# Performance work log

Measured on AMD Instinct MI355X. Metric: run time of the kernel, lower is better.

Reference implementation:

```python
import jax, jax.numpy as jnp
import numpy as np

D_MODEL = 512


def setup_inputs() -> dict:
    key = jax.random.key(0)
    ks = jax.random.split(key, 9)
    B, S, D = 2, 4096, D_MODEL
    scale = 1.0 / np.sqrt(D)
    return {
        "Q": jax.random.normal(ks[0], (B, S, D), dtype=jnp.float32),
        "K": jax.random.normal(ks[1], (B, S, D), dtype=jnp.float32),
        "V": jax.random.normal(ks[2], (B, S, D), dtype=jnp.float32),
        "W_q": jax.random.normal(ks[3], (D, D), dtype=jnp.float32) * scale,
        "b_q": jax.random.normal(ks[4], (D,), dtype=jnp.float32) * scale,
        "W_k": jax.random.normal(ks[5], (D, D), dtype=jnp.float32) * scale,
        "b_k": jax.random.normal(ks[6], (D,), dtype=jnp.float32) * scale,
        "W_v": jax.random.normal(ks[7], (D, D), dtype=jnp.float32) * scale,
        "b_v": jax.random.normal(ks[8], (D,), dtype=jnp.float32) * scale,
    }


def reference(Q, K, V, W_q, b_q, W_k, b_k, W_v, b_v):
    # Linear projections (torch Linear: x @ W.T + b)
    q = jnp.einsum("bsd,ed->bse", Q, W_q) + b_q  # [B,S,D]
    k = jnp.einsum("bsd,ed->bse", K, W_k) + b_k
    v = jnp.einsum("bsd,ed->bse", V, W_v) + b_v
    d_k = k.shape[-1]
    scores = jnp.einsum("bqd,bkd->bqk", q, k) / jnp.sqrt(jnp.asarray(d_k, q.dtype))
    attn = jax.nn.softmax(scores, axis=-1)  # [B,S,S]
    return jnp.einsum("bqk,bkd->bqd", attn, v)
```

## Files before the change

kernel.cpp:

```cpp
#include <hip/hip_runtime.h>
#include <hip/hip_bf16.h>
#include <math.h>
#include <stdint.h>

typedef __attribute__((ext_vector_type(8))) short short8;
typedef __attribute__((ext_vector_type(4))) float floatx4;
typedef __attribute__((ext_vector_type(4))) unsigned short ushort4v;

__device__ __forceinline__ void gload_lds16(const void* g, void* lds) {
    __builtin_amdgcn_global_load_lds(
        (__attribute__((address_space(1))) void*)(g),
        (__attribute__((address_space(3))) void*)(lds), 16, 0, 0);
}
__device__ __forceinline__ float bf16bits_to_f(unsigned short u) {
    union { unsigned int i; float f; } x; x.i = ((unsigned int)u) << 16; return x.f;
}
__device__ __forceinline__ unsigned short f_to_bf16bits(float f) {
    union { float f; unsigned int i; } x; x.f = f;
    unsigned int lsb = (x.i >> 16) & 1u;
    x.i += 0x7fffu + lsb;
    return (unsigned short)(x.i >> 16);
}

__global__ __launch_bounds__(256) void conv1_kernel(
    const float4* __restrict__ in, ushort4v* __restrict__ out)
{
    const int i = blockIdx.x * 256 + threadIdx.x;
    float4 v = in[i];
    ushort4v o;
    o[0] = f_to_bf16bits(v.x); o[1] = f_to_bf16bits(v.y);
    o[2] = f_to_bf16bits(v.z); o[3] = f_to_bf16bits(v.w);
    out[i] = o;
}

__global__ __launch_bounds__(256) void conv_wb_kernel(
    const float* __restrict__ Wq, const float* __restrict__ Wk, const float* __restrict__ Wv,
    const float* __restrict__ bq, const float* __restrict__ bk, const float* __restrict__ bv,
    unsigned short* __restrict__ Wo,
    unsigned short* __restrict__ bo)
{
    const int m = blockIdx.y;
    const float* W = (m == 0) ? Wq : (m == 1) ? Wk : Wv;
    const float* b = (m == 0) ? bq : (m == 1) ? bk : bv;
    if (blockIdx.x < 256) {
        const int idx = (blockIdx.x * 256 + threadIdx.x) * 4;
        float4 v = *(const float4*)&W[idx];
        ushort4v o;
        o[0] = f_to_bf16bits(v.x); o[1] = f_to_bf16bits(v.y);
        o[2] = f_to_bf16bits(v.z); o[3] = f_to_bf16bits(v.w);
        *(ushort4v*)&Wo[(size_t)m * 262144 + idx] = o;
    } else if (threadIdx.x < 128) {
        const int idx = threadIdx.x * 4;
        float4 v = *(const float4*)&b[idx];
        ushort4v o;
        o[0] = f_to_bf16bits(v.x); o[1] = f_to_bf16bits(v.y);
        o[2] = f_to_bf16bits(v.z); o[3] = f_to_bf16bits(v.w);
        *(ushort4v*)&bo[(size_t)m * 512 + idx] = o;
    }
}

__global__ __launch_bounds__(256, 2) void proj_kernel(
    const unsigned short* __restrict__ X,
    const unsigned short* __restrict__ W,
    const unsigned short* __restrict__ bias,
    unsigned short* __restrict__ qbuf,
    unsigned short* __restrict__ kbuf,
    unsigned short* __restrict__ vTbuf,
    int mode, float qscale)
{
    __shared__ __align__(16) unsigned short Xs[128 * 64];
    __shared__ __align__(16) unsigned short Ws[128 * 64];

    const int tid = threadIdx.x;
    const int wave = tid >> 6, lane = tid & 63, quad = lane >> 4, l15 = lane & 15;
    const int m0 = (int)(blockIdx.x >> 2) << 7;
    const int n0 = (int)(blockIdx.x & 3) << 7;
    const int mw = (wave >> 1) << 6, nw = (wave & 1) << 6;

    floatx4 acc[4][4];
    #pragma unroll
    for (int i = 0; i < 4; i++)
        #pragma unroll
        for (int j = 0; j < 4; j++) acc[i][j] = floatx4{0.f, 0.f, 0.f, 0.f};

    for (int kt = 0; kt < 512; kt += 64) {
        #pragma unroll
        for (int i = 0; i < 4; i++) {
            const int r0 = wave * 32 + i * 8;
            gload_lds16(X + (size_t)(m0 + r0 + (lane >> 3)) * 512 + kt + (lane & 7) * 8, &Xs[r0 * 64]);
            gload_lds16(W + (size_t)(n0 + r0 + (lane >> 3)) * 512 + kt + (lane & 7) * 8, &Ws[r0 * 64]);
        }
        __syncthreads();
        #pragma unroll
        for (int kk = 0; kk < 64; kk += 32) {
            short8 a[4], b[4];
            #pragma unroll
            for (int i = 0; i < 4; i++) a[i] = *(const short8*)&Xs[(mw + 16 * i + l15) * 64 + kk + quad * 8];
            #pragma unroll
            for (int j = 0; j < 4; j++) b[j] = *(const short8*)&Ws[(nw + 16 * j + l15) * 64 + kk + quad * 8];
            #pragma unroll
            for (int i = 0; i < 4; i++)
                #pragma unroll
                for (int j = 0; j < 4; j++)
                    acc[i][j] = __builtin_amdgcn_mfma_f32_16x16x32_bf16(a[i], b[j], acc[i][j], 0, 0, 0);
        }
        __syncthreads();
    }

    float bfj[4];
    #pragma unroll
    for (int j = 0; j < 4; j++) bfj[j] = bf16bits_to_f(bias[n0 + nw + 16 * j + l15]);

    if (mode < 2) {
        unsigned short* out = (mode == 0) ? qbuf : kbuf;
        const float s = (mode == 0) ? qscale : 1.0f;
        #pragma unroll
        for (int i = 0; i < 4; i++) {
            const int mrow = m0 + mw + 16 * i + quad * 4;
            #pragma unroll
            for (int j = 0; j < 4; j++) {
                const int n = n0 + nw + 16 * j + l15;
                #pragma unroll
                for (int r = 0; r < 4; r++)
                    out[(size_t)(mrow + r) * 512 + n] = f_to_bf16bits((acc[i][j][r] + bfj[j]) * s);
            }
        }
    } else {
        #pragma unroll
        for (int i = 0; i < 4; i++) {
            const int mrow = m0 + mw + 16 * i + quad * 4;
            const int bb = mrow >> 12;
            const int s4 = mrow & 4095;
            #pragma unroll
            for (int j = 0; j < 4; j++) {
                const int n = n0 + nw + 16 * j + l15;
                ushort4v pk;
                #pragma unroll
                for (int r = 0; r < 4; r++) pk[r] = f_to_bf16bits(acc[i][j][r] + bfj[j]);
                *(ushort4v*)&vTbuf[((size_t)bb * 512 + n) * 4096 + s4] = pk;
            }
        }
    }
}

template <int NSPLIT>
__global__ __launch_bounds__(256, 2) void attn_kernel(
    const unsigned short* __restrict__ q,
    const unsigned short* __restrict__ k,
    const unsigned short* __restrict__ vT,
    unsigned short* __restrict__ num,
    float* __restrict__ denom)
{
    constexpr int TK  = 32;
    constexpr int KST = 520;
    constexpr int PST = 40;
    __shared__ __align__(16) unsigned short Ks [TK * KST];
    __shared__ __align__(16) unsigned short Vts[512 * TK];
    __shared__ __align__(16) unsigned short Ps [64 * PST];

    const int tid = threadIdx.x;
    const int wave = tid >> 6, lane = tid & 63, quad = lane >> 4, l15 = lane & 15;
    const int bid = blockIdx.x;
    const int sp   = bid & (NSPLIT - 1);
    const int qblk = bid / NSPLIT;
    const int bb = qblk >> 6;
    const int q0 = (qblk & 63) << 6;
    const size_t rowbase = (size_t)bb * 4096 + q0;

    short8 qf[16];
    {
        const unsigned short* qrow = q + (rowbase + 16 * wave + l15) * 512;
        #pragma unroll
        for (int t = 0; t < 16; t++) qf[t] = *(const short8*)&qrow[t * 32 + quad * 8];
    }

    floatx4 oacc[4][8];
    #pragma unroll
    for (int i = 0; i < 4; i++)
        #pragma unroll
        for (int c = 0; c < 8; c++) oacc[i][c] = floatx4{0.f, 0.f, 0.f, 0.f};
    float dsum[4] = {0.f, 0.f, 0.f, 0.f};

    const unsigned short* kb = k  + (size_t)bb * 4096 * 512;
    const unsigned short* vb = vT + (size_t)bb * 512 * 4096;

    const int jbeg = sp * (4096 / NSPLIT);
    const int jend = jbeg + (4096 / NSPLIT);
    for (int j0 = jbeg; j0 < jend; j0 += TK) {
        #pragma unroll
        for (int r = 0; r < 8; r++) {
            const int row = wave * 8 + r;
            gload_lds16(kb + (size_t)(j0 + row) * 512 + lane * 8, &Ks[row * KST]);
        }
        #pragma unroll
        for (int i2 = 0; i2 < 8; i2++) {
            const int dd0 = (wave * 8 + i2) * 16;
            gload_lds16(vb + (size_t)(dd0 + (lane >> 2)) * 4096 + j0 + (lane & 3) * 8,
                        &Vts[dd0 * TK]);
        }
        __syncthreads();

        floatx4 sA[2], sB[2];
        sA[0] = sA[1] = sB[0] = sB[1] = floatx4{0.f, 0.f, 0.f, 0.f};
        #pragma unroll
        for (int t = 0; t < 16; t += 2) {
            #pragma unroll
            for (int c = 0; c < 2; c++) {
                short8 b0 = *(const short8*)&Ks[(c * 16 + l15) * KST + t * 32 + quad * 8];
                sA[c] = __builtin_amdgcn_mfma_f32_16x16x32_bf16(qf[t], b0, sA[c], 0, 0, 0);
                short8 b1 = *(const short8*)&Ks[(c * 16 + l15) * KST + (t + 1) * 32 + quad * 8];
                sB[c] = __builtin_amdgcn_mfma_f32_16x16x32_bf16(qf[t + 1], b1, sB[c], 0, 0, 0);
            }
        }
        #pragma unroll
        for (int c = 0; c < 2; c++) {
            #pragma unroll
            for (int r = 0; r < 4; r++) {
                const float p = __expf(fminf(sA[c][r] + sB[c][r], 30.0f));
                const unsigned short pb = f_to_bf16bits(p);
                dsum[r] += bf16bits_to_f(pb);
                Ps[(16 * wave + quad * 4 + r) * PST + c * 16 + l15] = pb;
            }
        }
        __syncthreads();

        short8 ap[4];
        #pragma unroll
        for (int i = 0; i < 4; i++) ap[i] = *(const short8*)&Ps[(16 * i + l15) * PST + quad * 8];
        #pragma unroll
        for (int c = 0; c < 8; c++) {
            short8 bvf = *(const short8*)&Vts[(128 * wave + 16 * c + l15) * TK + quad * 8];
            #pragma unroll
            for (int i = 0; i < 4; i++)
                oacc[i][c] = __builtin_amdgcn_mfma_f32_16x16x32_bf16(ap[i], bvf, oacc[i][c], 0, 0, 0);
        }
        __syncthreads();
    }

    #pragma unroll
    for (int r = 0; r < 4; r++) {
        float v = dsum[r];
        v += __shfl_xor(v, 1);
        v += __shfl_xor(v, 2);
        v += __shfl_xor(v, 4);
        v += __shfl_xor(v, 8);
        dsum[r] = v;
    }
    if (l15 == 0) {
        #pragma unroll
        for (int r = 0; r < 4; r++)
            denom[(size_t)sp * 8192 + rowbase + 16 * wave + quad * 4 + r] = dsum[r];
    }

    #pragma unroll
    for (int i = 0; i < 4; i++) {
        #pragma unroll
        for (int r = 0; r < 4; r++) {
            const size_t row = rowbase + 16 * i + quad * 4 + r;
            unsigned short* np_ = num + ((size_t)sp * 8192 + row) * 512 + 128 * wave + l15;
            #pragma unroll
            for (int c = 0; c < 8; c++)
                np_[16 * c] = f_to_bf16bits(oacc[i][c][r]);
        }
    }
}

__global__ __launch_bounds__(256) void combine_kernel(
    const unsigned short* __restrict__ num,
    const float* __restrict__ denom,
    float* __restrict__ out,
    int nsplit)
{
    const int gid = blockIdx.x * 256 + threadIdx.x;
    const int srow = gid >> 6;
    const int d0 = (gid & 63) << 3;
    float s[8];
    #pragma unroll
    for (int e = 0; e < 8; e++) s[e] = 0.f;
    float den = 0.f;
    for (int sp = 0; sp < nsplit; sp++) {
        den += denom[(size_t)sp * 8192 + srow];
        short8 v = *(const short8*)(num + ((size_t)sp * 8192 + srow) * 512 + d0);
        #pragma unroll
        for (int e = 0; e < 8; e++) s[e] += bf16bits_to_f((unsigned short)v[e]);
    }
    const float inv = 1.0f / den;
    float4 o0, o1;
    o0.x = s[0] * inv; o0.y = s[1] * inv; o0.z = s[2] * inv; o0.w = s[3] * inv;
    o1.x = s[4] * inv; o1.y = s[5] * inv; o1.z = s[6] * inv; o1.w = s[7] * inv;
    float* op = out + (size_t)srow * 512 + d0;
    *(float4*)op = o0;
    *(float4*)(op + 4) = o1;
}

extern "C" void kernel_launch(void* const* d_in, const int* in_sizes, int n_in,
                              void* d_out, int out_size, void* d_ws, size_t ws_size,
                              hipStream_t stream)
{
    (void)in_sizes; (void)n_in; (void)out_size;
    const float* Qin = (const float*)d_in[0];
    const float* Kin = (const float*)d_in[1];
    const float* Vin = (const float*)d_in[2];
    const float* Wq  = (const float*)d_in[3];
    const float* bq  = (const float*)d_in[4];
    const float* Wk  = (const float*)d_in[5];
    const float* bk  = (const float*)d_in[6];
    const float* Wv  = (const float*)d_in[7];
    const float* bv  = (const float*)d_in[8];

    const size_t M  = (size_t)8192 * 512;
    const size_t WS = (size_t)512 * 512;

    auto need = [&](size_t a_elems, int ns) -> size_t {
        return 2 * (a_elems + 3 * M + 3 * WS + 3 * 512) + 16 + (size_t)ns * 8192 * 4;
    };
    int nsplit; size_t a_elems; bool batched;
    if (ws_size >= need(4 * M, 4))      { nsplit = 4; a_elems = 4 * M; batched = true;  }
    else if (ws_size >= need(3 * M, 2)) { nsplit = 2; a_elems = 3 * M; batched = true;  }
    else                                { nsplit = 1; a_elems = 1 * M; batched = false; }

    unsigned short* ws   = (unsigned short*)d_ws;
    unsigned short* slotA = ws;
    unsigned short* qbuf  = ws + a_elems;
    unsigned short* kbuf  = qbuf + M;
    unsigned short* vTbuf = kbuf + M;
    unsigned short* Wc    = vTbuf + M;
    unsigned short* bc    = Wc + 3 * WS;
    size_t denom_off = (2 * (size_t)((bc + 3 * 512) - ws) + 15) & ~(size_t)15;
    float* denom = (float*)((char*)d_ws + denom_off);
    unsigned short* numb = slotA;

    const float qscale = 1.0f / sqrtf(512.0f);
    const float* Xin[3] = { Qin, Kin, Vin };

    conv_wb_kernel<<<dim3(257, 3), 256, 0, stream>>>(Wq, Wk, Wv, bq, bk, bv, Wc, bc);

    if (batched) {
        for (int m = 0; m < 3; m++)
            conv1_kernel<<<4096, 256, 0, stream>>>((const float4*)Xin[m],
                                                   (ushort4v*)(slotA + (size_t)m * M));
        for (int m = 0; m < 3; m++)
            proj_kernel<<<256, 256, 0, stream>>>(slotA + (size_t)m * M,
                                                 Wc + (size_t)m * WS, bc + (size_t)m * 512,
                                                 qbuf, kbuf, vTbuf, m, qscale);
    } else {
        for (int m = 0; m < 3; m++) {
            conv1_kernel<<<4096, 256, 0, stream>>>((const float4*)Xin[m], (ushort4v*)slotA);
            proj_kernel<<<256, 256, 0, stream>>>(slotA,
                                                 Wc + (size_t)m * WS, bc + (size_t)m * 512,
                                                 qbuf, kbuf, vTbuf, m, qscale);
        }
    }

    if (nsplit == 4)
        attn_kernel<4><<<dim3(512), dim3(256), 0, stream>>>(qbuf, kbuf, vTbuf, numb, denom);
    else if (nsplit == 2)
        attn_kernel<2><<<dim3(256), dim3(256), 0, stream>>>(qbuf, kbuf, vTbuf, numb, denom);
    else
        attn_kernel<1><<<dim3(128), dim3(256), 0, stream>>>(qbuf, kbuf, vTbuf, numb, denom);

    combine_kernel<<<dim3(2048), dim3(256), 0, stream>>>(
        numb, denom, (float*)d_out, nsplit);
}
```

Baseline: 265.5 us.

## Replace fused attention with materialized P GEMMs, atomics, and batched launches

Replaces the fused split-K attention kernel with two separate GEMM kernels. The first computes exp(QK^T) for a 2048-column chunk, writes the bf16 P matrix to workspace and accumulates row sums with atomics. The second multiplies P by V^T with a split-K of 2 and atomically accumulates into the fp32 output, which is then divided in place. It also merges the three conversion launches and three projection launches into single grid launches and removes the workspace-size fallbacks. The approach writes and rereads a large P matrix and adds heavy fp32 atomics on the output, in exchange for GEMM-style 128x128 tiling with better reuse.

```diff
diff --git a/kernel.cpp b/kernel.cpp
--- a/kernel.cpp
+++ b/kernel.cpp
@@ -22,15 +22,19 @@
     return (unsigned short)(x.i >> 16);
 }
 
-__global__ __launch_bounds__(256) void conv1_kernel(
-    const float4* __restrict__ in, ushort4v* __restrict__ out)
-{
-    const int i = blockIdx.x * 256 + threadIdx.x;
-    float4 v = in[i];
+__global__ __launch_bounds__(256) void conv_qkv_kernel(
+    const float* __restrict__ Q, const float* __restrict__ K, const float* __restrict__ V,
+    unsigned short* __restrict__ out)
+{
+    const int seg = blockIdx.x >> 12;
+    const int blk = blockIdx.x & 4095;
+    const float* src = (seg == 0) ? Q : (seg == 1) ? K : V;
+    const int idx = (blk * 256 + threadIdx.x) * 4;
+    float4 v = *(const float4*)&src[idx];
     ushort4v o;
     o[0] = f_to_bf16bits(v.x); o[1] = f_to_bf16bits(v.y);
     o[2] = f_to_bf16bits(v.z); o[3] = f_to_bf16bits(v.w);
-    out[i] = o;
+    *(ushort4v*)&out[(size_t)seg * 4194304 + idx] = o;
 }
 
 __global__ __launch_bounds__(256) void conv_wb_kernel(
@@ -60,16 +64,21 @@
 }
 
 __global__ __launch_bounds__(256, 2) void proj_kernel(
-    const unsigned short* __restrict__ X,
-    const unsigned short* __restrict__ W,
-    const unsigned short* __restrict__ bias,
+    const unsigned short* __restrict__ Xall,
+    const unsigned short* __restrict__ Wall,
+    const unsigned short* __restrict__ ball,
     unsigned short* __restrict__ qbuf,
     unsigned short* __restrict__ kbuf,
     unsigned short* __restrict__ vTbuf,
-    int mode, float qscale)
+    float qscale)
 {
     __shared__ __align__(16) unsigned short Xs[128 * 64];
     __shared__ __align__(16) unsigned short Ws[128 * 64];
+
+    const int mode = blockIdx.y;
+    const unsigned short* X = Xall + (size_t)mode * 4194304;
+    const unsigned short* W = Wall + (size_t)mode * 262144;
+    const unsigned short* bias = ball + (size_t)mode * 512;
 
     const int tid = threadIdx.x;
     const int wave = tid >> 6, lane = tid & 63, quad = lane >> 4, l15 = lane & 15;
@@ -143,161 +152,176 @@
     }
 }
 
-template <int NSPLIT>
-__global__ __launch_bounds__(256, 2) void attn_kernel(
-    const unsigned short* __restrict__ q,
-    const unsigned short* __restrict__ k,
-    const unsigned short* __restrict__ vT,
-    unsigned short* __restrict__ num,
-    float* __restrict__ denom)
-{
-    constexpr int TK  = 32;
-    constexpr int KST = 520;
-    constexpr int PST = 40;
-    __shared__ __align__(16) unsigned short Ks [TK * KST];
-    __shared__ __align__(16) unsigned short Vts[512 * TK];
-    __shared__ __align__(16) unsigned short Ps [64 * PST];
+__global__ __launch_bounds__(256, 2) void sgemm_exp_kernel(
+    const unsigned short* __restrict__ Aq,
+    const unsigned short* __restrict__ Bk,
+    unsigned short* __restrict__ P,
+    float* __restrict__ denom,
+    int coff)
+{
+    __shared__ __align__(16) unsigned short Xs[128 * 64];
+    __shared__ __align__(16) unsigned short Ws[128 * 64];
 
     const int tid = threadIdx.x;
     const int wave = tid >> 6, lane = tid & 63, quad = lane >> 4, l15 = lane & 15;
-    const int bid = blockIdx.x;
-    const int sp   = bid & (NSPLIT - 1);
-    const int qblk = bid / NSPLIT;
-    const int bb = qblk >> 6;
-    const int q0 = (qblk & 63) << 6;
-    const size_t rowbase = (size_t)bb * 4096 + q0;
-
-    short8 qf[16];
-    {
-        const unsigned short* qrow = q + (rowbase + 16 * wave + l15) * 512;
-        #pragma unroll
-        for (int t = 0; t < 16; t++) qf[t] = *(const short8*)&qrow[t * 32 + quad * 8];
-    }
-
-    floatx4 oacc[4][8];
+    const int rb = blockIdx.x >> 4, nb = blockIdx.x & 15;
+    const int m0 = rb << 7, n0 = nb << 7;
+    const int bb = m0 >> 12;
+    const int mw = (wave >> 1) << 6, nw = (wave & 1) << 6;
+
+    const unsigned short* Brow = Bk + ((size_t)(bb << 12) + coff + n0) * 512;
+
+    floatx4 acc[4][4];
     #pragma unroll
     for (int i = 0; i < 4; i++)
         #pragma unroll
-        for (int c = 0; c < 8; c++) oacc[i][c] = floatx4{0.f, 0.f, 0.f, 0.f};
-    float dsum[4] = {0.f, 0.f, 0.f, 0.f};
-
-    const unsigned short* kb = k  + (size_t)bb * 4096 * 512;
-    const unsigned short* vb = vT + (size_t)bb * 512 * 4096;
-
-    const int jbeg = sp * (4096 / NSPLIT);
-    const int jend = jbeg + (4096 / NSPLIT);
-    for (int j0 = jbeg; j0 < jend; j0 += TK) {
-        #pragma unroll
-        for (int r = 0; r < 8; r++) {
-            const int row = wave * 8 + r;
-            gload_lds16(kb + (size_t)(j0 + row) * 512 + lane * 8, &Ks[row * KST]);
-        }
-        #pragma unroll
-        for (int i2 = 0; i2 < 8; i2++) {
-            const int dd0 = (wave * 8 + i2) * 16;
-            gload_lds16(vb + (size_t)(dd0 + (lane >> 2)) * 4096 + j0 + (lane & 3) * 8,
-                        &Vts[dd0 * TK]);
-        }
-        __syncthreads();
-
-        floatx4 sA[2], sB[2];
-        sA[0] = sA[1] = sB[0] = sB[1] = floatx4{0.f, 0.f, 0.f, 0.f};
-        #pragma unroll
-        for (int t = 0; t < 16; t += 2) {
-            #pragma unroll
-            for (int c = 0; c < 2; c++) {
-                short8 b0 = *(const short8*)&Ks[(c * 16 + l15) * KST + t * 32 + quad * 8];
-                sA[c] = __builtin_amdgcn_mfma_f32_16x16x32_bf16(qf[t], b0, sA[c], 0, 0, 0);
-                short8 b1 = *(const short8*)&Ks[(c * 16 + l15) * KST + (t + 1) * 32 + quad * 8];
-                sB[c] = __builtin_amdgcn_mfma_f32_16x16x32_bf16(qf[t + 1], b1, sB[c], 0, 0, 0);
+        for (int j = 0; j < 4; j++) acc[i][j] = floatx4{0.f, 0.f, 0.f, 0.f};
+
+    for (int kt = 0; kt < 512; kt += 64) {
+        #pragma unroll
+        for (int i = 0; i < 4; i++) {
+            const int r0 = wave * 32 + i * 8;
+            gload_lds16(Aq + (size_t)(m0 + r0 + (lane >> 3)) * 512 + kt + (lane & 7) * 8, &Xs[r0 * 64]);
+            gload_lds16(Brow + (size_t)(r0 + (lane >> 3)) * 512 + kt + (lane & 7) * 8, &Ws[r0 * 64]);
+        }
+        __syncthreads();
+        #pragma unroll
+        for (int kk = 0; kk < 64; kk += 32) {
+            short8 a[4], b[4];
+            #pragma unroll
+            for (int i = 0; i < 4; i++) a[i] = *(const short8*)&Xs[(mw + 16 * i + l15) * 64 + kk + quad * 8];
+            #pragma unroll
+            for (int j = 0; j < 4; j++) b[j] = *(const short8*)&Ws[(nw + 16 * j + l15) * 64 + kk + quad * 8];
+            #pragma unroll
+            for (int i = 0; i < 4; i++)
+                #pragma unroll
+                for (int j = 0; j < 4; j++)
+                    acc[i][j] = __builtin_amdgcn_mfma_f32_16x16x32_bf16(a[i], b[j], acc[i][j], 0, 0, 0);
+        }
+        __syncthreads();
+    }
+
+    float rs[4][4];
+    #pragma unroll
+    for (int i = 0; i < 4; i++)
+        #pragma unroll
+        for (int r = 0; r < 4; r++) rs[i][r] = 0.f;
+
+    #pragma unroll
+    for (int i = 0; i < 4; i++) {
+        const int mrow = m0 + mw + 16 * i + quad * 4;
+        #pragma unroll
+        for (int j = 0; j < 4; j++) {
+            const int n = n0 + nw + 16 * j + l15;
+            #pragma unroll
+            for (int r = 0; r < 4; r++) {
+                const float p = __expf(fminf(acc[i][j][r], 30.0f));
+                const unsigned short pb = f_to_bf16bits(p);
+                P[(size_t)(mrow + r) * 2048 + n] = pb;
+                rs[i][r] += bf16bits_to_f(pb);
             }
         }
-        #pragma unroll
-        for (int c = 0; c < 2; c++) {
-            #pragma unroll
-            for (int r = 0; r < 4; r++) {
-                const float p = __expf(fminf(sA[c][r] + sB[c][r], 30.0f));
-                const unsigned short pb = f_to_bf16bits(p);
-                dsum[r] += bf16bits_to_f(pb);
-                Ps[(16 * wave + quad * 4 + r) * PST + c * 16 + l15] = pb;
-            }
-        }
-        __syncthreads();
-
-        short8 ap[4];
-        #pragma unroll
-        for (int i = 0; i < 4; i++) ap[i] = *(const short8*)&Ps[(16 * i + l15) * PST + quad * 8];
-        #pragma unroll
-        for (int c = 0; c < 8; c++) {
-            short8 bvf = *(const short8*)&Vts[(128 * wave + 16 * c + l15) * TK + quad * 8];
+    }
+    #pragma unroll
+    for (int i = 0; i < 4; i++) {
+        #pragma unroll
+        for (int r = 0; r < 4; r++) {
+            float v = rs[i][r];
+            v += __shfl_xor(v, 1);
+            v += __shfl_xor(v, 2);
+            v += __shfl_xor(v, 4);
+            v += __shfl_xor(v, 8);
+            if (l15 == 0)
+                atomicAdd(&denom[m0 + mw + 16 * i + quad * 4 + r], v);
+        }
+    }
+}
+
+__global__ __launch_bounds__(256, 2) void ogemm_kernel(
+    const unsigned short* __restrict__ P,
+    const unsigned short* __restrict__ vT,
+    float* __restrict__ onum,
+    int coff)
+{
+    __shared__ __align__(16) unsigned short Xs[128 * 64];
+    __shared__ __align__(16) unsigned short Ws[128 * 64];
+
+    const int tid = threadIdx.x;
+    const int wave = tid >> 6, lane = tid & 63, quad = lane >> 4, l15 = lane & 15;
+    const int rb = blockIdx.x >> 3;
+    const int nb = (blockIdx.x >> 1) & 3;
+    const int kss = blockIdx.x & 1;
+    const int m0 = rb << 7, n0 = nb << 7;
+    const int bb = m0 >> 12;
+    const int mw = (wave >> 1) << 6, nw = (wave & 1) << 6;
+
+    const unsigned short* Ab = P + (size_t)m0 * 2048 + (kss << 10);
+    const unsigned short* Bb = vT + (size_t)bb * 2097152 + (size_t)n0 * 4096 + coff + (kss << 10);
+
+    floatx4 acc[4][4];
+    #pragma unroll
+    for (int i = 0; i < 4; i++)
+        #pragma unroll
+        for (int j = 0; j < 4; j++) acc[i][j] = floatx4{0.f, 0.f, 0.f, 0.f};
+
+    for (int kt = 0; kt < 1024; kt += 64) {
+        #pragma unroll
+        for (int i = 0; i < 4; i++) {
+            const int r0 = wave * 32 + i * 8;
+            gload_lds16(Ab + (size_t)(r0 + (lane >> 3)) * 2048 + kt + (lane & 7) * 8, &Xs[r0 * 64]);
+            gload_lds16(Bb + (size_t)(r0 + (lane >> 3)) * 4096 + kt + (lane & 7) * 8, &Ws[r0 * 64]);
+        }
+        __syncthreads();
+        #pragma unroll
+        for (int kk = 0; kk < 64; kk += 32) {
+            short8 a[4], b[4];
+            #pragma unroll
+            for (int i = 0; i < 4; i++) a[i] = *(const short8*)&Xs[(mw + 16 * i + l15) * 64 + kk + quad * 8];
+            #pragma unroll
+            for (int j = 0; j < 4; j++) b[j] = *(const short8*)&Ws[(nw + 16 * j + l15) * 64 + kk + quad * 8];
             #pragma unroll
             for (int i = 0; i < 4; i++)
-                oacc[i][c] = __builtin_amdgcn_mfma_f32_16x16x32_bf16(ap[i], bvf, oacc[i][c], 0, 0, 0);
-        }
-        __syncthreads();
-    }
-
-    #pragma unroll
-    for (int r = 0; r < 4; r++) {
-        float v = dsum[r];
-        v += __shfl_xor(v, 1);
-        v += __shfl_xor(v, 2);
-        v += __shfl_xor(v, 4);
-        v += __shfl_xor(v, 8);
-        dsum[r] = v;
-    }
-    if (l15 == 0) {
-        #pragma unroll
-        for (int r = 0; r < 4; r++)
-            denom[(size_t)sp * 8192 + rowbase + 16 * wave + quad * 4 + r] = dsum[r];
+                #pragma unroll
+                for (int j = 0; j < 4; j++)
+                    acc[i][j] = __builtin_amdgcn_mfma_f32_16x16x32_bf16(a[i], b[j], acc[i][j], 0, 0, 0);
+        }
+        __syncthreads();
     }
 
     #pragma unroll
     for (int i = 0; i < 4; i++) {
-        #pragma unroll
-        for (int r = 0; r < 4; r++) {
-            const size_t row = rowbase + 16 * i + quad * 4 + r;
-            unsigned short* np_ = num + ((size_t)sp * 8192 + row) * 512 + 128 * wave + l15;
-            #pragma unroll
-            for (int c = 0; c < 8; c++)
-                np_[16 * c] = f_to_bf16bits(oacc[i][c][r]);
-        }
-    }
-}
-
-__global__ __launch_bounds__(256) void combine_kernel(
-    const unsigned short* __restrict__ num,
-    const float* __restrict__ denom,
-    float* __restrict__ out,
-    int nsplit)
+        const int mrow = m0 + mw + 16 * i + quad * 4;
+        #pragma unroll
+        for (int j = 0; j < 4; j++) {
+            const int n = n0 + nw + 16 * j + l15;
+            #pragma unroll
+            for (int r = 0; r < 4; r++)
+                atomicAdd(&onum[(size_t)(mrow + r) * 512 + n], acc[i][j][r]);
+        }
+    }
+}
+
+__global__ __launch_bounds__(256) void divide_kernel(
+    float* __restrict__ out, const float* __restrict__ denom)
 {
     const int gid = blockIdx.x * 256 + threadIdx.x;
-    const int srow = gid >> 6;
+    const int row = gid >> 6;
     const int d0 = (gid & 63) << 3;
-    float s[8];
-    #pragma unroll
-    for (int e = 0; e < 8; e++) s[e] = 0.f;
-    float den = 0.f;
-    for (int sp = 0; sp < nsplit; sp++) {
-        den += denom[(size_t)sp * 8192 + srow];
-        short8 v = *(const short8*)(num + ((size_t)sp * 8192 + srow) * 512 + d0);
-        #pragma unroll
-        for (int e = 0; e < 8; e++) s[e] += bf16bits_to_f((unsigned short)v[e]);
-    }
-    const float inv = 1.0f / den;
-    float4 o0, o1;
-    o0.x = s[0] * inv; o0.y = s[1] * inv; o0.z = s[2] * inv; o0.w = s[3] * inv;
-    o1.x = s[4] * inv; o1.y = s[5] * inv; o1.z = s[6] * inv; o1.w = s[7] * inv;
-    float* op = out + (size_t)srow * 512 + d0;
-    *(float4*)op = o0;
-    *(float4*)(op + 4) = o1;
+    const float inv = 1.0f / denom[row];
+    float* p = out + (size_t)row * 512 + d0;
+    float4 a = *(float4*)p;
+    float4 b = *(float4*)(p + 4);
+    a.x *= inv; a.y *= inv; a.z *= inv; a.w *= inv;
+    b.x *= inv; b.y *= inv; b.z *= inv; b.w *= inv;
+    *(float4*)p = a;
+    *(float4*)(p + 4) = b;
 }
 
 extern "C" void kernel_launch(void* const* d_in, const int* in_sizes, int n_in,
                               void* d_out, int out_size, void* d_ws, size_t ws_size,
                               hipStream_t stream)
 {
-    (void)in_sizes; (void)n_in; (void)out_size;
+    (void)in_sizes; (void)n_in; (void)out_size; (void)ws_size;
     const float* Qin = (const float*)d_in[0];
     const float* Kin = (const float*)d_in[1];
     const float* Vin = (const float*)d_in[2];
@@ -308,57 +332,35 @@
     const float* Wv  = (const float*)d_in[7];
     const float* bv  = (const float*)d_in[8];
 
-    const size_t M  = (size_t)8192 * 512;
-    const size_t WS = (size_t)512 * 512;
-
-    auto need = [&](size_t a_elems, int ns) -> size_t {
-        return 2 * (a_elems + 3 * M + 3 * WS + 3 * 512) + 16 + (size_t)ns * 8192 * 4;
-    };
-    int nsplit; size_t a_elems; bool batched;
-    if (ws_size >= need(4 * M, 4))      { nsplit = 4; a_elems = 4 * M; batched = true;  }
-    else if (ws_size >= need(3 * M, 2)) { nsplit = 2; a_elems = 3 * M; batched = true;  }
-    else                                { nsplit = 1; a_elems = 1 * M; batched = false; }
+    const size_t M   = 4194304;
+    const size_t PCH = 16777216;
+    const size_t WS_ = 262144;
 
     unsigned short* ws   = (unsigned short*)d_ws;
-    unsigned short* slotA = ws;
-    unsigned short* qbuf  = ws + a_elems;
-    unsigned short* kbuf  = qbuf + M;
-    unsigned short* vTbuf = kbuf + M;
-    unsigned short* Wc    = vTbuf + M;
-    unsigned short* bc    = Wc + 3 * WS;
-    size_t denom_off = (2 * (size_t)((bc + 3 * 512) - ws) + 15) & ~(size_t)15;
-    float* denom = (float*)((char*)d_ws + denom_off);
-    unsigned short* numb = slotA;
+    unsigned short* A    = ws;
+    unsigned short* qs   = ws + PCH;
+    unsigned short* ks   = qs + M;
+    unsigned short* vT   = ks + M;
+    unsigned short* Wc   = vT + M;
+    unsigned short* bc   = Wc + 3 * WS_;
+    float* denom = (float*)(((uintptr_t)(bc + 3 * 512) + 15) & ~(uintptr_t)15);
+    float* onum  = (float*)d_out;
 
     const float qscale = 1.0f / sqrtf(512.0f);
-    const float* Xin[3] = { Qin, Kin, Vin };
-
-    conv_wb_kernel<<<dim3(257, 3), 256, 0, stream>>>(Wq, Wk, Wv, bq, bk, bv, Wc, bc);
-
-    if (batched) {
-        for (int m = 0; m < 3; m++)
-            conv1_kernel<<<4096, 256, 0, stream>>>((const float4*)Xin[m],
-                                                   (ushort4v*)(slotA + (size_t)m * M));
-        for (int m = 0; m < 3; m++)
-            proj_kernel<<<256, 256, 0, stream>>>(slotA + (size_t)m * M,
-                                                 Wc + (size_t)m * WS, bc + (size_t)m * 512,
-                                                 qbuf, kbuf, vTbuf, m, qscale);
-    } else {
-        for (int m = 0; m < 3; m++) {
-            conv1_kernel<<<4096, 256, 0, stream>>>((const float4*)Xin[m], (ushort4v*)slotA);
-            proj_kernel<<<256, 256, 0, stream>>>(slotA,
-                                                 Wc + (size_t)m * WS, bc + (size_t)m * 512,
-                                                 qbuf, kbuf, vTbuf, m, qscale);
-        }
-    }
-
-    if (nsplit == 4)
-        attn_kernel<4><<<dim3(512), dim3(256), 0, stream>>>(qbuf, kbuf, vTbuf, numb, denom);
-    else if (nsplit == 2)
-        attn_kernel<2><<<dim3(256), dim3(256), 0, stream>>>(qbuf, kbuf, vTbuf, numb, denom);
-    else
-        attn_kernel<1><<<dim3(128), dim3(256), 0, stream>>>(qbuf, kbuf, vTbuf, numb, denom);
-
-    combine_kernel<<<dim3(2048), dim3(256), 0, stream>>>(
-        numb, denom, (float*)d_out, nsplit);
-}
+
+    conv_qkv_kernel<<<dim3(3 * 4096), dim3(256), 0, stream>>>(Qin, Kin, Vin, A);
+    conv_wb_kernel<<<dim3(257, 3), dim3(256), 0, stream>>>(Wq, Wk, Wv, bq, bk, bv, Wc, bc);
+
+    hipMemsetAsync(denom, 0, 8192 * sizeof(float), stream);
+    hipMemsetAsync(onum, 0, (size_t)8192 * 512 * sizeof(float), stream);
+
+    proj_kernel<<<dim3(256, 3), dim3(256), 0, stream>>>(A, Wc, bc, qs, ks, vT, qscale);
+
+    for (int c = 0; c < 2; c++) {
+        const int coff = c * 2048;
+        sgemm_exp_kernel<<<dim3(1024), dim3(256), 0, stream>>>(qs, ks, A, denom, coff);
+        ogemm_kernel<<<dim3(512), dim3(256), 0, stream>>>(A, vT, onum, coff);
+    }
+
+    divide_kernel<<<dim3(2048), dim3(256), 0, stream>>>(onum, denom);
+}
```

Measured after the change: 311.8 us. 1.17x slower.
